# Kernel optimization log

Measured on AMD Instinct MI355X. Metric: run time of the kernel, lower is better.

The kernel has to match this reference:

```python
import jax, jax.numpy as jnp
import numpy as np

B, D, H, NB = 4096, 2048, 2048, 4
BIN, BOUT = D // NB, H // NB
EPS = 1e-5


def _block_linear(x, W, b):
    # x: [B, nb*bin], W: [nb, bin, bout], b: [nb, bout] -> [B, nb*bout]
    xr = x.reshape(x.shape[0], NB, BIN)
    y = jnp.einsum('bni,nio->bno', xr, W) + b
    return y.reshape(x.shape[0], NB * BOUT)


def setup_inputs() -> dict:
    key = jax.random.key(0)
    ks = jax.random.split(key, 24)
    sW = 1.0 / np.sqrt(BIN)
    sR = 1.0 / np.sqrt(BOUT)
    inp = {
        'x': jax.random.normal(ks[0], (B, D), jnp.float32),
        'h_prev': jax.random.normal(ks[1], (B, H), jnp.float32),
        'c_prev': jax.random.normal(ks[2], (B, H), jnp.float32),
        'ln_g': jnp.ones((D,), jnp.float32),
        'ln_b': jnp.zeros((D,), jnp.float32),
        'conv_w': jax.random.normal(ks[3], (3,), jnp.float32) * 0.5,
        'conv_b': jnp.zeros((), jnp.float32),
    }
    names = ['Wz', 'Wi', 'Wf', 'Wo']
    for j, n in enumerate(names):
        inp[n] = jax.random.normal(ks[4 + j], (NB, BIN, BOUT), jnp.float32) * sW
        inp['b' + n[1]] = jax.random.normal(ks[8 + j], (NB, BOUT), jnp.float32) * sW
    rnames = ['Rz', 'Ri', 'Rf', 'Ro']
    for j, n in enumerate(rnames):
        inp[n] = jax.random.normal(ks[12 + j], (NB, BOUT, BOUT), jnp.float32) * sR
        inp['rb' + n[1]] = jax.random.normal(ks[16 + j], (NB, BOUT), jnp.float32) * sR
    return inp


def reference(x, h_prev, c_prev, ln_g, ln_b, conv_w, conv_b,
              Wz, bz, Wi, bi, Wf, bf, Wo, bo,
              Rz, rbz, Ri, rbi, Rf, rbf, Ro, rbo):
    # LayerNorm over the feature dim
    mu = jnp.mean(x, axis=-1, keepdims=True)
    var = jnp.mean((x - mu) ** 2, axis=-1, keepdims=True)
    x_norm = (x - mu) * jax.lax.rsqrt(var + EPS) * ln_g + ln_b

    # Causal conv1d (kernel 3) along the feature axis, then SiLU
    xp = jnp.pad(x_norm, ((0, 0), (2, 0)))  # left-pad 2 -> causal
    xc = conv_w[0] * xp[:, :D] + conv_w[1] * xp[:, 1:D + 1] + conv_w[2] * xp[:, 2:D + 2] + conv_b
    x_conv = jax.nn.silu(xc)

    z = jnp.tanh(_block_linear(x, Wz, bz) + _block_linear(h_prev, Rz, rbz))
    i = jax.nn.sigmoid(_block_linear(x_conv, Wi, bi) + _block_linear(h_prev, Ri, rbi))
    f = jax.nn.sigmoid(_block_linear(x_conv, Wf, bf) + _block_linear(h_prev, Rf, rbf))
    o = jax.nn.sigmoid(_block_linear(x, Wo, bo) + _block_linear(h_prev, Ro, rbo))

    c_t = f * c_prev + i * z
    h_t = o * jnp.tanh(c_t)
    return (h_t, c_t)
```

## Files before the change

kernel.cpp:

```cpp
#include <hip/hip_runtime.h>
#include <hip/hip_bf16.h>
#include <math.h>

#define BB 4096
#define DD 2048
#define HH 2048

typedef __bf16 bf16x8 __attribute__((ext_vector_type(8)));
typedef float f32x4 __attribute__((ext_vector_type(4)));

__device__ __forceinline__ void async16(const void* g, void* l) {
  __builtin_amdgcn_global_load_lds(
      (const __attribute__((address_space(1))) unsigned int*)g,
      (__attribute__((address_space(3))) unsigned int*)l,
      16, 0, 0);
}

__device__ __forceinline__ float sigmoidf_(float x) {
  return 1.0f / (1.0f + __expf(-x));
}

__device__ __forceinline__ void store_bf8(__hip_bfloat16* dst, const float* v) {
  union { __hip_bfloat16 b[8]; uint4 u; } p;
#pragma unroll
  for (int e = 0; e < 8; e++) p.b[e] = __float2bfloat16(v[e]);
  *(uint4*)dst = p.u;
}

__global__ void prep_bias(const float* __restrict__ bz, const float* __restrict__ bi,
                          const float* __restrict__ bf, const float* __restrict__ bo,
                          const float* __restrict__ rbz, const float* __restrict__ rbi,
                          const float* __restrict__ rbf, const float* __restrict__ rbo,
                          float* __restrict__ bias) {
  int i = blockIdx.x * 256 + threadIdx.x;
  if (i < 2048) {
    bias[0 * 2048 + i] = bz[i] + rbz[i];
    bias[1 * 2048 + i] = bi[i] + rbi[i];
    bias[2 * 2048 + i] = bf[i] + rbf[i];
    bias[3 * 2048 + i] = bo[i] + rbo[i];
  }
}

__global__ __launch_bounds__(256) void prep_w(
    const float* __restrict__ Wz, const float* __restrict__ Wi,
    const float* __restrict__ Wf, const float* __restrict__ Wo,
    const float* __restrict__ Rz, const float* __restrict__ Ri,
    const float* __restrict__ Rf, const float* __restrict__ Ro,
    __hip_bfloat16* __restrict__ WT2) {
  const int jt = blockIdx.x;
  const int ksg = blockIdx.y;
  const int gn = blockIdx.z;
  const int g = gn >> 2, nn = gn & 3;
  const int kg0 = ksg * 128;
  const float* src;
  int krow;
  if (kg0 < 512) { src = (g == 0 ? Wz : g == 1 ? Wi : g == 2 ? Wf : Wo); krow = kg0; }
  else           { src = (g == 0 ? Rz : g == 1 ? Ri : g == 2 ? Rf : Ro); krow = kg0 - 512; }
  const int j0 = jt * 32;
  __shared__ float tile[128][33];
  const int t = threadIdx.x;
  const int jj = t & 31, kk0 = (t >> 5) * 16;
  const float* s0 = src + ((size_t)nn * 512 + krow + kk0) * 512 + j0 + jj;
#pragma unroll
  for (int rr = 0; rr < 16; rr++) tile[kk0 + rr][jj] = s0[(size_t)rr * 512];
  __syncthreads();
#pragma unroll
  for (int q = 0; q < 2; q++) {
    int u = t + q * 256;
    int ksl = u >> 7, j = (u >> 2) & 31, pc = u & 3;
    int c = pc ^ ((j >> 1) & 3);
    float v[8];
#pragma unroll
    for (int e = 0; e < 8; e++) v[e] = tile[ksl * 32 + c * 8 + e][j];
    size_t gr = ((size_t)(gn * 16 + jt) * 32 + ksg * 4 + ksl) * 128 + j * 4 + pc;
    store_bf8(WT2 + gr * 8, v);
  }
}

__global__ __launch_bounds__(256) void prep_act(
    const float* __restrict__ x, const float* __restrict__ h,
    const float* __restrict__ lg, const float* __restrict__ lb,
    const float* __restrict__ cw, const float* __restrict__ cb,
    __hip_bfloat16* __restrict__ xh2, __hip_bfloat16* __restrict__ xc2) {
  const int r = blockIdx.x, t = threadIdx.x, l = t & 63;
  const int mb = r >> 7, rl = r & 127, swz = (rl >> 1) & 3;
  const int n = t >> 6, ktl = (t >> 2) & 15, pc = (t & 3) ^ swz;
  __shared__ float red[8];
  __shared__ float edge[256][2];
  const float* xr = x + (size_t)r * 2048;
  const float* hr = h + (size_t)r * 2048;
  float4 v0 = ((const float4*)xr)[t * 2];
  float4 v1 = ((const float4*)xr)[t * 2 + 1];
  float vv[8] = {v0.x, v0.y, v0.z, v0.w, v1.x, v1.y, v1.z, v1.w};
  float s = 0.f, s2 = 0.f;
#pragma unroll
  for (int e = 0; e < 8; e++) { s += vv[e]; s2 += vv[e] * vv[e]; }
#pragma unroll
  for (int off = 32; off > 0; off >>= 1) {
    s += __shfl_down(s, off);
    s2 += __shfl_down(s2, off);
  }
  const int w = t >> 6;
  if (l == 0) { red[w] = s; red[4 + w] = s2; }
  __syncthreads();
  const float mu = (red[0] + red[1] + red[2] + red[3]) * (1.0f / 2048.0f);
  const float var = (red[4] + red[5] + red[6] + red[7]) * (1.0f / 2048.0f) - mu * mu;
  const float rs = rsqrtf(var + 1e-5f);

  float4 h0 = ((const float4*)hr)[t * 2];
  float4 h1 = ((const float4*)hr)[t * 2 + 1];
  float hh[8] = {h0.x, h0.y, h0.z, h0.w, h1.x, h1.y, h1.z, h1.w};
  float4 g0 = ((const float4*)lg)[t * 2], g1 = ((const float4*)lg)[t * 2 + 1];
  float4 b0 = ((const float4*)lb)[t * 2], b1 = ((const float4*)lb)[t * 2 + 1];
  float gg[8] = {g0.x, g0.y, g0.z, g0.w, g1.x, g1.y, g1.z, g1.w};
  float bb[8] = {b0.x, b0.y, b0.z, b0.w, b1.x, b1.y, b1.z, b1.w};
  float fr[8];
#pragma unroll
  for (int e = 0; e < 8; e++) fr[e] = (vv[e] - mu) * rs * gg[e] + bb[e];

  const size_t bx = ((size_t)(mb * 4 + n) * 32 + ktl) * 512 + rl * 4 + pc;
  const size_t bh = ((size_t)(mb * 4 + n) * 32 + 16 + ktl) * 512 + rl * 4 + pc;
  store_bf8(xh2 + bx * 8, vv);
  store_bf8(xh2 + bh * 8, hh);

  edge[t][0] = fr[6]; edge[t][1] = fr[7];
  __syncthreads();
  float p6 = __shfl_up(fr[6], 1);
  float p7 = __shfl_up(fr[7], 1);
  if (l == 0) {
    p6 = (t > 0) ? edge[t - 1][0] : 0.f;
    p7 = (t > 0) ? edge[t - 1][1] : 0.f;
  }
  const float w0 = cw[0], w1 = cw[1], w2 = cw[2], cbv = cb[0];
  float sc[8];
  {
    float xc0 = w0 * p6 + w1 * p7 + w2 * fr[0] + cbv;
    float xc1 = w0 * p7 + w1 * fr[0] + w2 * fr[1] + cbv;
    sc[0] = xc0 * sigmoidf_(xc0);
    sc[1] = xc1 * sigmoidf_(xc1);
  }
#pragma unroll
  for (int e = 2; e < 8; e++) {
    float xc = w0 * fr[e - 2] + w1 * fr[e - 1] + w2 * fr[e] + cbv;
    sc[e] = xc * sigmoidf_(xc);
  }
  const size_t bc = ((size_t)(mb * 4 + n) * 16 + ktl) * 512 + rl * 4 + pc;
  store_bf8(xc2 + bc * 8, sc);
}

__global__ __launch_bounds__(256, 4) void gemm_fused(
    const __hip_bfloat16* __restrict__ xh2, const __hip_bfloat16* __restrict__ xc2,
    const __hip_bfloat16* __restrict__ WT2, const float* __restrict__ bias,
    const float* __restrict__ c_prev, float* __restrict__ out) {
  __shared__ __attribute__((aligned(16))) char smem[24576];
  __hip_bfloat16* As1 = (__hip_bfloat16*)smem;
  __hip_bfloat16* As2 = (__hip_bfloat16*)(smem + 8192);
  __hip_bfloat16* Bs  = (__hip_bfloat16*)(smem + 16384);
  __hip_bfloat16* zo  = (__hip_bfloat16*)smem;

  const int mb = blockIdx.x, jt = blockIdx.y, n = blockIdx.z;
  const int t = threadIdx.x, w = t >> 6, l = t & 63;
  const int pair = w >> 1, mhalf = w & 1;
  const int lj = l & 15;

  const char* pA = (const char*)xh2 + (size_t)(mb * 4 + n) * 262144 + t * 16;
  const char* pC = (const char*)xc2 + (size_t)(mb * 4 + n) * 131072 + t * 16;
  const int gate1 = t >> 7;
  const char* pB1 = (const char*)WT2 + (size_t)((gate1 * 4 + n) * 16 + jt) * 65536 + (t & 127) * 16;
  const char* pB2 = (const char*)WT2 + (size_t)(((gate1 + 2) * 4 + n) * 16 + jt) * 65536 + (t & 127) * 16;
  char* dA1 = (char*)As1 + t * 16;
  char* dC1 = (char*)As2 + t * 16;
  char* dB1 = (char*)Bs + t * 16;

  const int fo = lj * 64 + (((l >> 4) ^ ((lj >> 1) & 3)) * 16);
  const int g0 = pair ? 1 : 0, g1 = pair ? 2 : 3;

  f32x4 acc[4][2][2] = {};

  for (int ks = 0; ks < 32; ++ks) {
    __syncthreads();
    async16(pA, dA1);
    async16(pA + 4096, dA1 + 4096);
    if (ks < 16) {
      async16(pC, dC1);
      async16(pC + 4096, dC1 + 4096);
    }
    async16(pB1, dB1);
    async16(pB2, dB1 + 4096);
    pA += 8192; pC += 8192; pB1 += 2048; pB2 += 2048;
    __syncthreads();

    const char* Ab = (pair == 1 && ks < 16) ? (const char*)As2 : (const char*)As1;
    Ab += mhalf * 4096 + fo;
    bf16x8 af[4];
#pragma unroll
    for (int s = 0; s < 4; ++s) af[s] = *(const bf16x8*)(Ab + s * 1024);
    const char* Bb = (const char*)Bs + fo;
#pragma unroll
    for (int sj = 0; sj < 2; ++sj) {
      bf16x8 b0 = *(const bf16x8*)(Bb + g0 * 2048 + sj * 1024);
      bf16x8 b1 = *(const bf16x8*)(Bb + g1 * 2048 + sj * 1024);
#pragma unroll
      for (int s = 0; s < 4; ++s) {
        acc[s][sj][0] = __builtin_amdgcn_mfma_f32_16x16x32_bf16(af[s], b0, acc[s][sj][0], 0, 0, 0);
        acc[s][sj][1] = __builtin_amdgcn_mfma_f32_16x16x32_bf16(af[s], b1, acc[s][sj][1], 0, 0, 0);
      }
    }
  }

  const int r0 = (l >> 4) * 4;
  const int colb = n * 512 + jt * 32;
  __syncthreads();
  if (pair == 0) {
#pragma unroll
    for (int sj = 0; sj < 2; ++sj) {
      const int jc = sj * 16 + lj;
      const float bz_ = bias[colb + jc];
      const float bo_ = bias[3 * 2048 + colb + jc];
#pragma unroll
      for (int s = 0; s < 4; ++s) {
#pragma unroll
        for (int rr = 0; rr < 4; ++rr) {
          const int rl = mhalf * 64 + s * 16 + r0 + rr;
          zo[rl * 36 + jc] = __float2bfloat16(tanhf(acc[s][sj][0][rr] + bz_));
          zo[(128 + rl) * 36 + jc] = __float2bfloat16(sigmoidf_(acc[s][sj][1][rr] + bo_));
        }
      }
    }
  }
  __syncthreads();
  if (pair == 1) {
    const size_t HC = (size_t)BB * HH;
#pragma unroll
    for (int sj = 0; sj < 2; ++sj) {
      const int jc = sj * 16 + lj;
      const int col = colb + jc;
      const float bi_ = bias[1 * 2048 + col];
      const float bf_ = bias[2 * 2048 + col];
#pragma unroll
      for (int s = 0; s < 4; ++s) {
#pragma unroll
        for (int rr = 0; rr < 4; ++rr) {
          const int rl = mhalf * 64 + s * 16 + r0 + rr;
          const int row = mb * 128 + rl;
          const float z  = __bfloat162float(zo[rl * 36 + jc]);
          const float og = __bfloat162float(zo[(128 + rl) * 36 + jc]);
          const float ig = sigmoidf_(acc[s][sj][0][rr] + bi_);
          const float fg = sigmoidf_(acc[s][sj][1][rr] + bf_);
          const float cp = c_prev[(size_t)row * 2048 + col];
          const float c = fg * cp + ig * z;
          const float hv = og * tanhf(c);
          out[(size_t)row * 2048 + col] = hv;
          out[HC + (size_t)row * 2048 + col] = c;
        }
      }
    }
  }
}

extern "C" void kernel_launch(void* const* d_in, const int* in_sizes, int n_in,
                              void* d_out, int out_size, void* d_ws, size_t ws_size,
                              hipStream_t stream) {
  const float* x      = (const float*)d_in[0];
  const float* h_prev = (const float*)d_in[1];
  const float* c_prev = (const float*)d_in[2];
  const float* ln_g   = (const float*)d_in[3];
  const float* ln_b   = (const float*)d_in[4];
  const float* conv_w = (const float*)d_in[5];
  const float* conv_b = (const float*)d_in[6];
  const float* Wz = (const float*)d_in[7];
  const float* bz = (const float*)d_in[8];
  const float* Wi = (const float*)d_in[9];
  const float* bi = (const float*)d_in[10];
  const float* Wf = (const float*)d_in[11];
  const float* bf = (const float*)d_in[12];
  const float* Wo = (const float*)d_in[13];
  const float* bo = (const float*)d_in[14];
  const float* Rz = (const float*)d_in[15];
  const float* rbz = (const float*)d_in[16];
  const float* Ri = (const float*)d_in[17];
  const float* rbi = (const float*)d_in[18];
  const float* Rf = (const float*)d_in[19];
  const float* rbf = (const float*)d_in[20];
  const float* Ro = (const float*)d_in[21];
  const float* rbo = (const float*)d_in[22];
  float* out = (float*)d_out;

  char* ws = (char*)d_ws;
  __hip_bfloat16* xh2 = (__hip_bfloat16*)(ws);
  __hip_bfloat16* xc2 = (__hip_bfloat16*)(ws + 33554432);
  __hip_bfloat16* WT2 = (__hip_bfloat16*)(ws + 33554432 + 16777216);
  float* bias         = (float*)(ws + 33554432 + 2 * 16777216);

  prep_bias<<<8, 256, 0, stream>>>(bz, bi, bf, bo, rbz, rbi, rbf, rbo, bias);
  prep_w<<<dim3(16, 8, 16), 256, 0, stream>>>(Wz, Wi, Wf, Wo, Rz, Ri, Rf, Ro, WT2);
  prep_act<<<BB, 256, 0, stream>>>(x, h_prev, ln_g, ln_b, conv_w, conv_b, xh2, xc2);
  gemm_fused<<<dim3(32, 16, 4), 256, 0, stream>>>(xh2, xc2, WT2, bias, c_prev, out);
}
```

Baseline: 355.7 us.

## Widen GEMM tile to 64 columns with 512 threads and double K step

The fused gate GEMM now has 512-thread blocks, each covering 64 output columns instead of 32 and loading twice the K depth per barrier. This halves A-operand reloads across column tiles and halves the number of sync iterations, at the cost of 64KB of LDS per block and lower occupancy. The weight prep kernel drops its shared-memory transpose and reads strided global memory directly, and tanhf is replaced by a fast exp-based version.

```diff
diff --git a/kernel.cpp b/kernel.cpp
--- a/kernel.cpp
+++ b/kernel.cpp
@@ -18,6 +18,10 @@
 
 __device__ __forceinline__ float sigmoidf_(float x) {
   return 1.0f / (1.0f + __expf(-x));
+}
+__device__ __forceinline__ float tanhf_(float x) {
+  float t = __expf(-2.0f * fabsf(x));
+  return copysignf((1.0f - t) / (1.0f + t), x);
 }
 
 __device__ __forceinline__ void store_bf8(__hip_bfloat16* dst, const float* v) {
@@ -51,27 +55,20 @@
   const int ksg = blockIdx.y;
   const int gn = blockIdx.z;
   const int g = gn >> 2, nn = gn & 3;
-  const int kg0 = ksg * 128;
   const float* src;
-  int krow;
-  if (kg0 < 512) { src = (g == 0 ? Wz : g == 1 ? Wi : g == 2 ? Wf : Wo); krow = kg0; }
-  else           { src = (g == 0 ? Rz : g == 1 ? Ri : g == 2 ? Rf : Ro); krow = kg0 - 512; }
-  const int j0 = jt * 32;
-  __shared__ float tile[128][33];
+  if (ksg < 4) src = (g == 0 ? Wz : g == 1 ? Wi : g == 2 ? Wf : Wo);
+  else         src = (g == 0 ? Rz : g == 1 ? Ri : g == 2 ? Rf : Ro);
   const int t = threadIdx.x;
-  const int jj = t & 31, kk0 = (t >> 5) * 16;
-  const float* s0 = src + ((size_t)nn * 512 + krow + kk0) * 512 + j0 + jj;
-#pragma unroll
-  for (int rr = 0; rr < 16; rr++) tile[kk0 + rr][jj] = s0[(size_t)rr * 512];
-  __syncthreads();
 #pragma unroll
   for (int q = 0; q < 2; q++) {
     int u = t + q * 256;
     int ksl = u >> 7, j = (u >> 2) & 31, pc = u & 3;
     int c = pc ^ ((j >> 1) & 3);
+    int kr = (ksg & 3) * 128 + ksl * 32 + c * 8;
+    const float* s0 = src + ((size_t)nn * 512 + kr) * 512 + jt * 32 + j;
     float v[8];
 #pragma unroll
-    for (int e = 0; e < 8; e++) v[e] = tile[ksl * 32 + c * 8 + e][j];
+    for (int e = 0; e < 8; e++) v[e] = s0[(size_t)e * 512];
     size_t gr = ((size_t)(gn * 16 + jt) * 32 + ksg * 4 + ksl) * 128 + j * 4 + pc;
     store_bf8(WT2 + gr * 8, v);
   }
@@ -148,73 +145,73 @@
   store_bf8(xc2 + bc * 8, sc);
 }
 
-__global__ __launch_bounds__(256, 4) void gemm_fused(
+__global__ __launch_bounds__(512, 4) void gemm_fused(
     const __hip_bfloat16* __restrict__ xh2, const __hip_bfloat16* __restrict__ xc2,
     const __hip_bfloat16* __restrict__ WT2, const float* __restrict__ bias,
     const float* __restrict__ c_prev, float* __restrict__ out) {
-  __shared__ __attribute__((aligned(16))) char smem[24576];
-  __hip_bfloat16* As1 = (__hip_bfloat16*)smem;
-  __hip_bfloat16* As2 = (__hip_bfloat16*)(smem + 8192);
-  __hip_bfloat16* Bs  = (__hip_bfloat16*)(smem + 16384);
-  __hip_bfloat16* zo  = (__hip_bfloat16*)smem;
+  __shared__ __attribute__((aligned(16))) char smem[65536];
+  __hip_bfloat16* zo = (__hip_bfloat16*)smem;
 
   const int mb = blockIdx.x, jt = blockIdx.y, n = blockIdx.z;
   const int t = threadIdx.x, w = t >> 6, l = t & 63;
-  const int pair = w >> 1, mhalf = w & 1;
+  const int pair = w >> 2, mhalf = (w >> 1) & 1, jhalf = w & 1;
   const int lj = l & 15;
 
   const char* pA = (const char*)xh2 + (size_t)(mb * 4 + n) * 262144 + t * 16;
   const char* pC = (const char*)xc2 + (size_t)(mb * 4 + n) * 131072 + t * 16;
-  const int gate1 = t >> 7;
-  const char* pB1 = (const char*)WT2 + (size_t)((gate1 * 4 + n) * 16 + jt) * 65536 + (t & 127) * 16;
-  const char* pB2 = (const char*)WT2 + (size_t)(((gate1 + 2) * 4 + n) * 16 + jt) * 65536 + (t & 127) * 16;
-  char* dA1 = (char*)As1 + t * 16;
-  char* dC1 = (char*)As2 + t * 16;
-  char* dB1 = (char*)Bs + t * 16;
+  const char* pB = (const char*)WT2 +
+      (size_t)(n * 16 + jt * 2 + ((t >> 8) & 1)) * 65536 + ((t >> 7) & 1) * 2048 + (t & 127) * 16;
+  char* dA = smem + t * 16;
+  char* dB = smem + 32768 + t * 16;
 
   const int fo = lj * 64 + (((l >> 4) ^ ((lj >> 1) & 3)) * 16);
   const int g0 = pair ? 1 : 0, g1 = pair ? 2 : 3;
 
   f32x4 acc[4][2][2] = {};
 
-  for (int ks = 0; ks < 32; ++ks) {
+  for (int ks2 = 0; ks2 < 16; ++ks2) {
     __syncthreads();
-    async16(pA, dA1);
-    async16(pA + 4096, dA1 + 4096);
-    if (ks < 16) {
-      async16(pC, dC1);
-      async16(pC + 4096, dC1 + 4096);
-    }
-    async16(pB1, dB1);
-    async16(pB2, dB1 + 4096);
-    pA += 8192; pC += 8192; pB1 += 2048; pB2 += 2048;
+    async16(pA, dA);
+    async16(pA + 8192, dA + 8192);
+    if (ks2 < 8) {
+      async16(pC, dA + 16384);
+      async16(pC + 8192, dA + 24576);
+    }
+    async16(pB, dB);
+    async16(pB + 4194304, dB + 8192);
+    async16(pB + 8388608, dB + 16384);
+    async16(pB + 12582912, dB + 24576);
+    pA += 16384; pC += 16384; pB += 4096;
     __syncthreads();
 
-    const char* Ab = (pair == 1 && ks < 16) ? (const char*)As2 : (const char*)As1;
-    Ab += mhalf * 4096 + fo;
-    bf16x8 af[4];
-#pragma unroll
-    for (int s = 0; s < 4; ++s) af[s] = *(const bf16x8*)(Ab + s * 1024);
-    const char* Bb = (const char*)Bs + fo;
+    const char* Ab = ((ks2 < 8 && pair) ? smem + 16384 : smem) + mhalf * 4096 + fo;
+    const char* Bb = smem + 32768 + jhalf * 4096 + fo;
+#pragma unroll
+    for (int kh = 0; kh < 2; ++kh) {
+      bf16x8 af[4];
+#pragma unroll
+      for (int s = 0; s < 4; ++s)
+        af[s] = *(const bf16x8*)(Ab + kh * 8192 + s * 1024);
+#pragma unroll
+      for (int sj = 0; sj < 2; ++sj) {
+        bf16x8 b0 = *(const bf16x8*)(Bb + g0 * 8192 + kh * 2048 + sj * 1024);
+        bf16x8 b1 = *(const bf16x8*)(Bb + g1 * 8192 + kh * 2048 + sj * 1024);
+#pragma unroll
+        for (int s = 0; s < 4; ++s) {
+          acc[s][sj][0] = __builtin_amdgcn_mfma_f32_16x16x32_bf16(af[s], b0, acc[s][sj][0], 0, 0, 0);
+          acc[s][sj][1] = __builtin_amdgcn_mfma_f32_16x16x32_bf16(af[s], b1, acc[s][sj][1], 0, 0, 0);
+        }
+      }
+    }
+  }
+
+  const int r0 = (l >> 4) * 4;
+  const int colb = n * 512 + jt * 64;
+  __syncthreads();
+  if (pair == 0) {
 #pragma unroll
     for (int sj = 0; sj < 2; ++sj) {
-      bf16x8 b0 = *(const bf16x8*)(Bb + g0 * 2048 + sj * 1024);
-      bf16x8 b1 = *(const bf16x8*)(Bb + g1 * 2048 + sj * 1024);
-#pragma unroll
-      for (int s = 0; s < 4; ++s) {
-        acc[s][sj][0] = __builtin_amdgcn_mfma_f32_16x16x32_bf16(af[s], b0, acc[s][sj][0], 0, 0, 0);
-        acc[s][sj][1] = __builtin_amdgcn_mfma_f32_16x16x32_bf16(af[s], b1, acc[s][sj][1], 0, 0, 0);
-      }
-    }
-  }
-
-  const int r0 = (l >> 4) * 4;
-  const int colb = n * 512 + jt * 32;
-  __syncthreads();
-  if (pair == 0) {
-#pragma unroll
-    for (int sj = 0; sj < 2; ++sj) {
-      const int jc = sj * 16 + lj;
+      const int jc = jhalf * 32 + sj * 16 + lj;
       const float bz_ = bias[colb + jc];
       const float bo_ = bias[3 * 2048 + colb + jc];
 #pragma unroll
@@ -222,8 +219,8 @@
 #pragma unroll
         for (int rr = 0; rr < 4; ++rr) {
           const int rl = mhalf * 64 + s * 16 + r0 + rr;
-          zo[rl * 36 + jc] = __float2bfloat16(tanhf(acc[s][sj][0][rr] + bz_));
-          zo[(128 + rl) * 36 + jc] = __float2bfloat16(sigmoidf_(acc[s][sj][1][rr] + bo_));
+          zo[rl * 72 + jc] = __float2bfloat16(tanhf_(acc[s][sj][0][rr] + bz_));
+          zo[(128 + rl) * 72 + jc] = __float2bfloat16(sigmoidf_(acc[s][sj][1][rr] + bo_));
         }
       }
     }
@@ -233,7 +230,7 @@
     const size_t HC = (size_t)BB * HH;
 #pragma unroll
     for (int sj = 0; sj < 2; ++sj) {
-      const int jc = sj * 16 + lj;
+      const int jc = jhalf * 32 + sj * 16 + lj;
       const int col = colb + jc;
       const float bi_ = bias[1 * 2048 + col];
       const float bf_ = bias[2 * 2048 + col];
@@ -243,13 +240,13 @@
         for (int rr = 0; rr < 4; ++rr) {
           const int rl = mhalf * 64 + s * 16 + r0 + rr;
           const int row = mb * 128 + rl;
-          const float z  = __bfloat162float(zo[rl * 36 + jc]);
-          const float og = __bfloat162float(zo[(128 + rl) * 36 + jc]);
+          const float z  = __bfloat162float(zo[rl * 72 + jc]);
+          const float og = __bfloat162float(zo[(128 + rl) * 72 + jc]);
           const float ig = sigmoidf_(acc[s][sj][0][rr] + bi_);
           const float fg = sigmoidf_(acc[s][sj][1][rr] + bf_);
           const float cp = c_prev[(size_t)row * 2048 + col];
           const float c = fg * cp + ig * z;
-          const float hv = og * tanhf(c);
+          const float hv = og * tanhf_(c);
           out[(size_t)row * 2048 + col] = hv;
           out[HC + (size_t)row * 2048 + col] = c;
         }
@@ -295,5 +292,5 @@
   prep_bias<<<8, 256, 0, stream>>>(bz, bi, bf, bo, rbz, rbi, rbf, rbo, bias);
   prep_w<<<dim3(16, 8, 16), 256, 0, stream>>>(Wz, Wi, Wf, Wo, Rz, Ri, Rf, Ro, WT2);
   prep_act<<<BB, 256, 0, stream>>>(x, h_prev, ln_g, ln_b, conv_w, conv_b, xh2, xc2);
-  gemm_fused<<<dim3(32, 16, 4), 256, 0, stream>>>(xh2, xc2, WT2, bias, c_prev, out);
-}
+  gemm_fused<<<dim3(32, 8, 4), 512, 0, stream>>>(xh2, xc2, WT2, bias, c_prev, out);
+}
```

After: 334.2 us. -6.0%, faster.
